# Kernel tuning notes

Measured on AMD Instinct MI355X. Metric: run time of the kernel, lower is better.

Reference implementation:

```python
import jax, jax.numpy as jnp
import numpy as np

DMODEL = 1024
NUM_HEADS = 16
HEAD_DIM = DMODEL // NUM_HEADS


def setup_inputs() -> dict:
    key = jax.random.key(0)
    k_x, k_wqkv, k_bqkv, k_wo, k_bo = jax.random.split(key, 5)
    B, T, D = 4, 2048, DMODEL
    s = 1.0 / np.sqrt(D)
    return {
        "x": jax.random.normal(k_x, (B, T, D), dtype=jnp.float32),
        "w_qkv": jax.random.uniform(k_wqkv, (D, 3 * D), dtype=jnp.float32, minval=-s, maxval=s),
        "b_qkv": jax.random.uniform(k_bqkv, (3 * D,), dtype=jnp.float32, minval=-s, maxval=s),
        "w_out": jax.random.uniform(k_wo, (D, D), dtype=jnp.float32, minval=-s, maxval=s),
        "b_out": jax.random.uniform(k_bo, (D,), dtype=jnp.float32, minval=-s, maxval=s),
    }


def reference(x, w_qkv, b_qkv, w_out, b_out):
    B, T, D = x.shape
    H, Hd = NUM_HEADS, HEAD_DIM
    qkv = x @ w_qkv + b_qkv                      # [B,T,3D]
    qkv = qkv.reshape(B, T, 3, H, Hd)
    q = jnp.transpose(qkv[:, :, 0], (0, 2, 1, 3))  # [B,H,T,Hd]
    k = jnp.transpose(qkv[:, :, 1], (0, 2, 1, 3))
    v = jnp.transpose(qkv[:, :, 2], (0, 2, 1, 3))
    scores = jnp.einsum("bhqd,bhkd->bhqk", q, k) / jnp.sqrt(jnp.float32(Hd))
    weights = jax.nn.softmax(scores, axis=-1)
    attn = jnp.einsum("bhqk,bhkd->bhqd", weights, v)  # [B,H,T,Hd]
    attn = jnp.transpose(attn, (0, 2, 1, 3)).reshape(B, T, D)
    return attn @ w_out + b_out
```

## Files before the change

kernel.cpp:

```cpp
#include <hip/hip_runtime.h>
#include <hip/hip_bf16.h>


typedef __bf16 bf16_t;
typedef __bf16 bf16x8 __attribute__((ext_vector_type(8)));
typedef float f32x4 __attribute__((ext_vector_type(4)));
typedef short short4v __attribute__((ext_vector_type(4)));

#if __has_builtin(__builtin_amdgcn_mfma_f32_16x16x16_bf16)
typedef __bf16 bf16x4 __attribute__((ext_vector_type(4)));
#define MFMA_PV(va, vb, c) __builtin_amdgcn_mfma_f32_16x16x16_bf16( \
    __builtin_bit_cast(bf16x4, (va)), __builtin_bit_cast(bf16x4, (vb)), (c), 0, 0, 0)
#else
#define MFMA_PV(va, vb, c) __builtin_amdgcn_mfma_f32_16x16x16bf16_1k((va), (vb), (c), 0, 0, 0)
#endif

#define DMODEL 1024
#define NH     16
#define HD     64
#define BATCH  4
#define SEQ    2048
#define NTOK   (BATCH * SEQ)
#define NOUT   (NTOK * DMODEL)
#define CEXP   0.1803368801111204f

__device__ __forceinline__ void async_ld16(void* lds, const void* g) {
  __builtin_amdgcn_global_load_lds(
      (const __attribute__((address_space(1))) void*)g,
      (__attribute__((address_space(3))) void*)lds, 16, 0, 0);
}

__global__ __launch_bounds__(256) void sniff_dtype(
    const uint4* __restrict__ x, int* __restrict__ flag) {
  int t = threadIdx.x;
  uint4 v = x[t];
  int nanish = 0, zc = 0;
  for (int j = 0; j < 4; ++j) {
    uint4 w = x[t + j * 256];
    unsigned u[4] = {w.x, w.y, w.z, w.w};
    for (int k = 0; k < 4; ++k) {
      unsigned lo = u[k] & 0xFFFFu, hi = u[k] >> 16;
      if ((lo & 0x7F80u) == 0x7F80u) nanish++;
      if ((hi & 0x7F80u) == 0x7F80u) nanish++;
      if (lo == 0) zc++;
      if (hi == 0) zc++;
    }
  }
  (void)v;
  __shared__ int rn[256], rz[256];
  rn[t] = nanish; rz[t] = zc;
  __syncthreads();
  for (int s = 128; s > 0; s >>= 1) {
    if (t < s) { rn[t] += rn[t + s]; rz[t] += rz[t + s]; }
    __syncthreads();
  }
  if (t == 0) flag[0] = (rn[0] > 4 || rz[0] > 2048) ? 1 : 0;
}

__global__ __launch_bounds__(256) void conv_to_bf16(
    const void* __restrict__ src, bf16_t* __restrict__ dst, int n,
    const int* __restrict__ flag) {
  int i = (blockIdx.x * 256 + threadIdx.x) * 8;
  if (i >= n) return;
  if (flag[0]) {
    const float4* s = (const float4*)((const float*)src + i);
    float4 a = s[0], b = s[1];
    bf16_t* o = dst + i;
    o[0] = (bf16_t)a.x; o[1] = (bf16_t)a.y; o[2] = (bf16_t)a.z; o[3] = (bf16_t)a.w;
    o[4] = (bf16_t)b.x; o[5] = (bf16_t)b.y; o[6] = (bf16_t)b.z; o[7] = (bf16_t)b.w;
  } else {
    *(uint4*)(dst + i) = *(const uint4*)((const bf16_t*)src + i);
  }
}

__global__ __launch_bounds__(256) void conv_biases(
    const void* __restrict__ sq, const void* __restrict__ so,
    float* __restrict__ dq, float* __restrict__ dofs,
    const int* __restrict__ flag) {
  int i = blockIdx.x * 256 + threadIdx.x;
  if (i < 3072)
    dq[i] = flag[0] ? ((const float*)sq)[i] : (float)((const bf16_t*)sq)[i];
  else {
    int j = i - 3072;
    dofs[j] = flag[0] ? ((const float*)so)[j] : (float)((const bf16_t*)so)[j];
  }
}

__global__ __launch_bounds__(256) void transpose_w(
    const void* __restrict__ in, bf16_t* __restrict__ out, int R, int C,
    const int* __restrict__ flag) {
  __shared__ bf16_t tile[32][33];
  const int tx = threadIdx.x & 31, ty = threadIdx.x >> 5;
  const int c0 = blockIdx.x * 32, r0 = blockIdx.y * 32;
  if (flag[0]) {
    for (int i = 0; i < 4; ++i) {
      int r = ty + i * 8;
      tile[r][tx] = (bf16_t)((const float*)in)[(size_t)(r0 + r) * C + c0 + tx];
    }
  } else {
    for (int i = 0; i < 4; ++i) {
      int r = ty + i * 8;
      tile[r][tx] = ((const bf16_t*)in)[(size_t)(r0 + r) * C + c0 + tx];
    }
  }
  __syncthreads();
  for (int i = 0; i < 4; ++i) {
    int r = ty + i * 8;
    out[(size_t)(c0 + r) * R + r0 + tx] = tile[tx][r];
  }
}

template <int MODE>
__global__ __launch_bounds__(256) void gemm_bt_bias(
    const bf16_t* __restrict__ A, const bf16_t* __restrict__ Bt,
    const float* __restrict__ bias, void* __restrict__ Cout,
    int M, int N, int K, const int* __restrict__ flag,
    bf16_t* __restrict__ vT) {
  __shared__ bf16_t sA[128 * 32];
  __shared__ bf16_t sB[128 * 32];
  const int t = threadIdx.x;
  const int wave = t >> 6, lane = t & 63;
  const int quad = lane >> 4, l16 = lane & 15;
  const int bM = blockIdx.y * 128, bN = blockIdx.x * 128;
  const int m0w = (wave >> 1) * 64, n0w = (wave & 1) * 64;
  const int rowS = wave * 16 + (lane >> 2);
  const int kcS = (lane & 3) * 8;

  f32x4 acc[4][4] = {};

  for (int k0 = 0; k0 < K; k0 += 32) {
    for (int r = 0; r < 2; ++r) {
      int row = r * 64 + rowS;
      async_ld16((char*)sA + r * 4096 + wave * 1024,
                 A + (size_t)(bM + row) * K + k0 + kcS);
      async_ld16((char*)sB + r * 4096 + wave * 1024,
                 Bt + (size_t)(bN + row) * K + k0 + kcS);
    }
    __syncthreads();

    bf16x8 af[4], bfr[4];
    for (int i = 0; i < 4; ++i)
      af[i] = *(const bf16x8*)&sA[(m0w + i * 16 + l16) * 32 + quad * 8];
    for (int j = 0; j < 4; ++j)
      bfr[j] = *(const bf16x8*)&sB[(n0w + j * 16 + l16) * 32 + quad * 8];
    for (int i = 0; i < 4; ++i)
      for (int j = 0; j < 4; ++j)
        acc[i][j] = __builtin_amdgcn_mfma_f32_16x16x32_bf16(af[i], bfr[j], acc[i][j], 0, 0, 0);
    __syncthreads();
  }

  const bool f32out = (MODE == 1) && flag[0];
  for (int j = 0; j < 4; ++j) {
    int col = bN + n0w + j * 16 + l16;
    float bv = bias[col];
    for (int i = 0; i < 4; ++i) {
      int row0 = bM + m0w + i * 16 + quad * 4;
      if (MODE == 2 && col >= 2048) {
        int hh = (col - 2048) >> 6, dd = (col - 2048) & 63;
        bf16_t o4[4];
        for (int r = 0; r < 4; ++r) o4[r] = (bf16_t)(acc[i][j][r] + bv);
        size_t dst = ((((size_t)(row0 >> 11) * NH + hh) * HD + dd) << 11) | (row0 & 2047);
        *(uint2*)&vT[dst] = *(uint2*)o4;
      } else {
        float scale = (MODE == 2 && col < 1024) ? CEXP : 1.0f;
        for (int r = 0; r < 4; ++r) {
          float v = (acc[i][j][r] + bv) * scale;
          if (f32out) ((float*)Cout)[(size_t)(row0 + r) * N + col] = v;
          else        ((bf16_t*)Cout)[(size_t)(row0 + r) * N + col] = (bf16_t)v;
        }
      }
    }
  }
}

__global__ __launch_bounds__(512) void attention_v9(
    const bf16_t* __restrict__ qkv, const bf16_t* __restrict__ vT,
    bf16_t* __restrict__ attn) {
  const int t = threadIdx.x;
  const int wave = t >> 6, lane = t & 63;
  const int quad = lane >> 4, l16 = lane & 15;
  const int bh = blockIdx.x, b = bh >> 4, h = bh & 15;
  const int qw = blockIdx.y * 256 + wave * 32;

  __shared__ bf16_t Kt[2][128 * 64];
  __shared__ bf16_t Vt[2][64 * 128];

  const bf16_t* qglob = qkv + (size_t)b * SEQ * 3072 + h * 64;
  const bf16_t* kglob = qglob + 1024;
  const bf16_t* vglob = vT + (size_t)bh * HD * SEQ;

  bf16x8 qf[2][2];
  for (int s = 0; s < 2; ++s) {
    const bf16_t* qrow = qglob + (size_t)(qw + s * 16 + l16) * 3072 + quad * 8;
    qf[s][0] = *(const bf16x8*)qrow;
    qf[s][1] = *(const bf16x8*)(qrow + 32);
  }

  f32x4 accO[2][4] = {};
  float lpart[2] = {0.f, 0.f};

  const int kRow = lane >> 3, kSlot = lane & 7;
  const int vRow = lane >> 4, vSlot = lane & 15;

  auto stageKV = [&](int buf, int kt) {
    for (int j = 0; j < 2; ++j) {
      int keyl = wave * 16 + j * 8 + kRow;
      int gc = kSlot ^ (keyl & 7);
      async_ld16((char*)Kt[buf] + (wave * 16 + j * 8) * 128,
                 kglob + (size_t)(kt + keyl) * 3072 + gc * 8);
    }
    for (int j = 0; j < 2; ++j) {
      int d = wave * 8 + j * 4 + vRow;
      int gc = vSlot ^ (d & 15);
      async_ld16((char*)Vt[buf] + (wave * 8 + j * 4) * 256,
                 vglob + (size_t)d * SEQ + kt + gc * 8);
    }
  };

  stageKV(0, 0);

  for (int ti = 0; ti < SEQ / 128; ++ti) {
    const int buf = ti & 1;
    __syncthreads();
    if (ti + 1 < SEQ / 128) stageKV(buf ^ 1, (ti + 1) * 128);

    const bf16_t* KtB = Kt[buf];
    const bf16_t* VtB = Vt[buf];

    for (int kb = 0; kb < 8; ++kb) {
      const bf16_t* kr = &KtB[(kb * 16 + l16) * 64];
      bf16x8 kf0 = *(const bf16x8*)(kr + ((quad ^ (l16 & 7)) * 8));
      bf16x8 kf1 = *(const bf16x8*)(kr + (((4 + quad) ^ (l16 & 7)) * 8));

      short4v pB[2];
      for (int s = 0; s < 2; ++s) {
        f32x4 z = {0.f, 0.f, 0.f, 0.f};
        f32x4 st = __builtin_amdgcn_mfma_f32_16x16x32_bf16(kf0, qf[s][0], z, 0, 0, 0);
        st = __builtin_amdgcn_mfma_f32_16x16x32_bf16(kf1, qf[s][1], st, 0, 0, 0);
        union { bf16_t hh[4]; short4v s4; } u;
        for (int r = 0; r < 4; ++r) {
          float p = __builtin_amdgcn_exp2f(st[r]);
          lpart[s] += p;
          u.hh[r] = (bf16_t)p;
        }
        pB[s] = u.s4;
      }

      const int chunkbase = kb * 2 + (quad >> 1);
      const int coff = (quad & 1) * 4;
      for (int db = 0; db < 4; ++db) {
        short4v vf = *(const short4v*)&VtB[(db * 16 + l16) * 128 +
                                           ((chunkbase ^ l16) * 8) + coff];
        for (int s = 0; s < 2; ++s)
          accO[s][db] = MFMA_PV(vf, pB[s], accO[s][db]);
      }
    }
  }

  for (int s = 0; s < 2; ++s) {
    float l = lpart[s];
    l += __shfl_xor(l, 16);
    l += __shfl_xor(l, 32);
    float inv = 1.f / l;
    size_t tok = (size_t)b * SEQ + qw + s * 16 + l16;
    for (int db = 0; db < 4; ++db) {
      bf16_t o4[4];
      for (int r = 0; r < 4; ++r) o4[r] = (bf16_t)(accO[s][db][r] * inv);
      *(uint2*)&attn[tok * DMODEL + h * HD + db * 16 + quad * 4] = *(uint2*)o4;
    }
  }
}

extern "C" void kernel_launch(void* const* d_in, const int* in_sizes, int n_in,
                              void* d_out, int out_size, void* d_ws, size_t ws_size,
                              hipStream_t stream) {
  const void* x     = d_in[0];
  const void* w_qkv = d_in[1];
  const void* b_qkv = d_in[2];
  const void* w_out = d_in[3];
  const void* b_out = d_in[4];

  char* ws = (char*)d_ws;
  int*    flag  = (int*)ws;
  bf16_t* wqkvT = (bf16_t*)(ws + 4096);
  bf16_t* woutT = (bf16_t*)(ws + 6295552);
  float*  bqkvf = (float*)(ws + 8392704);
  float*  boutf = (float*)(ws + 8404992);
  bf16_t* qkv   = (bf16_t*)(ws + 8409088);
  bf16_t* xb    = (bf16_t*)(ws + 58740736);
  bf16_t* attn  = xb;
  bf16_t* vTbuf = (bf16_t*)(ws + 75517952);

  sniff_dtype<<<1, 256, 0, stream>>>((const uint4*)x, flag);

  conv_to_bf16<<<NOUT / 2048, 256, 0, stream>>>(x, xb, NOUT, flag);
  conv_biases<<<16, 256, 0, stream>>>(b_qkv, b_out, bqkvf, boutf, flag);

  transpose_w<<<dim3(96, 32), 256, 0, stream>>>(w_qkv, wqkvT, 1024, 3072, flag);
  transpose_w<<<dim3(32, 32), 256, 0, stream>>>(w_out, woutT, 1024, 1024, flag);

  gemm_bt_bias<2><<<dim3(24, 64), 256, 0, stream>>>(
      xb, wqkvT, bqkvf, qkv, NTOK, 3072, 1024, flag, vTbuf);

  attention_v9<<<dim3(BATCH * NH, SEQ / 256), 512, 0, stream>>>(qkv, vTbuf, attn);

  gemm_bt_bias<1><<<dim3(8, 64), 256, 0, stream>>>(
      attn, woutT, boutf, d_out, NTOK, 1024, 1024, flag, nullptr);
}
```

Measured before the change: 295.4 us.

## Software-pipeline QK and PV MFMAs in attention and swizzle GEMM block order

The attention inner loop is restructured so the QK^T scores for the next key block are computed while the exp and PV MFMAs of the current block run. Each wave starts at a different key sub-block to spread LDS bank traffic, s_setprio is raised around the PV MFMAs, and the row-sum is kept in four independent partial accumulators. Separately, the GEMM remaps workgroup IDs into eight strided groups, presumably to match XCD placement and improve L2 reuse. The pipelining costs extra registers, which could hurt occupancy.

```diff
diff --git a/kernel.cpp b/kernel.cpp
--- a/kernel.cpp
+++ b/kernel.cpp
@@ -121,7 +121,12 @@
   const int t = threadIdx.x;
   const int wave = t >> 6, lane = t & 63;
   const int quad = lane >> 4, l16 = lane & 15;
-  const int bM = blockIdx.y * 128, bN = blockIdx.x * 128;
+  const int nwg = gridDim.x * gridDim.y;
+  const int lin = blockIdx.y * gridDim.x + blockIdx.x;
+  const int cpx = nwg >> 3;
+  const int swz = (lin & 7) * cpx + (lin >> 3);
+  const int bx = swz % gridDim.x, by = swz / gridDim.x;
+  const int bM = by * 128, bN = bx * 128;
   const int m0w = (wave >> 1) * 64, n0w = (wave & 1) * 64;
   const int rowS = wave * 16 + (lane >> 2);
   const int kcS = (lane & 3) * 8;
@@ -173,7 +178,7 @@
   }
 }
 
-__global__ __launch_bounds__(512) void attention_v9(
+__global__ __launch_bounds__(512) void attention_v10(
     const bf16_t* __restrict__ qkv, const bf16_t* __restrict__ vT,
     bf16_t* __restrict__ attn) {
   const int t = threadIdx.x;
@@ -197,7 +202,7 @@
   }
 
   f32x4 accO[2][4] = {};
-  float lpart[2] = {0.f, 0.f};
+  f32x4 lp[2] = {};
 
   const int kRow = lane >> 3, kSlot = lane & 7;
   const int vRow = lane >> 4, vSlot = lane & 15;
@@ -219,6 +224,8 @@
 
   stageKV(0, 0);
 
+  const int kb0 = wave & 7;
+
   for (int ti = 0; ti < SEQ / 128; ++ti) {
     const int buf = ti & 1;
     __syncthreads();
@@ -227,38 +234,62 @@
     const bf16_t* KtB = Kt[buf];
     const bf16_t* VtB = Vt[buf];
 
-    for (int kb = 0; kb < 8; ++kb) {
-      const bf16_t* kr = &KtB[(kb * 16 + l16) * 64];
-      bf16x8 kf0 = *(const bf16x8*)(kr + ((quad ^ (l16 & 7)) * 8));
-      bf16x8 kf1 = *(const bf16x8*)(kr + (((4 + quad) ^ (l16 & 7)) * 8));
-
+    f32x4 stc[2];
+    {
+      const bf16_t* kr = &KtB[(kb0 * 16 + l16) * 64];
+      bf16x8 a = *(const bf16x8*)(kr + ((quad ^ (l16 & 7)) * 8));
+      bf16x8 c = *(const bf16x8*)(kr + (((4 + quad) ^ (l16 & 7)) * 8));
+      for (int s = 0; s < 2; ++s) {
+        f32x4 z = {0.f, 0.f, 0.f, 0.f};
+        stc[s] = __builtin_amdgcn_mfma_f32_16x16x32_bf16(a, qf[s][0], z, 0, 0, 0);
+        stc[s] = __builtin_amdgcn_mfma_f32_16x16x32_bf16(c, qf[s][1], stc[s], 0, 0, 0);
+      }
+    }
+
+#pragma unroll
+    for (int i = 0; i < 8; ++i) {
+      const int kbc = (kb0 + i) & 7;
+      bf16x8 an, cn;
+      if (i < 7) {
+        const int kbn = (kb0 + i + 1) & 7;
+        const bf16_t* kr = &KtB[(kbn * 16 + l16) * 64];
+        an = *(const bf16x8*)(kr + ((quad ^ (l16 & 7)) * 8));
+        cn = *(const bf16x8*)(kr + (((4 + quad) ^ (l16 & 7)) * 8));
+      }
       short4v pB[2];
       for (int s = 0; s < 2; ++s) {
-        f32x4 z = {0.f, 0.f, 0.f, 0.f};
-        f32x4 st = __builtin_amdgcn_mfma_f32_16x16x32_bf16(kf0, qf[s][0], z, 0, 0, 0);
-        st = __builtin_amdgcn_mfma_f32_16x16x32_bf16(kf1, qf[s][1], st, 0, 0, 0);
         union { bf16_t hh[4]; short4v s4; } u;
         for (int r = 0; r < 4; ++r) {
-          float p = __builtin_amdgcn_exp2f(st[r]);
-          lpart[s] += p;
+          float p = __builtin_amdgcn_exp2f(stc[s][r]);
+          lp[s][r] += p;
           u.hh[r] = (bf16_t)p;
         }
         pB[s] = u.s4;
       }
-
-      const int chunkbase = kb * 2 + (quad >> 1);
+      f32x4 stn[2];
+      if (i < 7) {
+        for (int s = 0; s < 2; ++s) {
+          f32x4 z = {0.f, 0.f, 0.f, 0.f};
+          stn[s] = __builtin_amdgcn_mfma_f32_16x16x32_bf16(an, qf[s][0], z, 0, 0, 0);
+          stn[s] = __builtin_amdgcn_mfma_f32_16x16x32_bf16(cn, qf[s][1], stn[s], 0, 0, 0);
+        }
+      }
+      const int chunkbase = kbc * 2 + (quad >> 1);
       const int coff = (quad & 1) * 4;
+      __builtin_amdgcn_s_setprio(1);
       for (int db = 0; db < 4; ++db) {
         short4v vf = *(const short4v*)&VtB[(db * 16 + l16) * 128 +
                                            ((chunkbase ^ l16) * 8) + coff];
         for (int s = 0; s < 2; ++s)
           accO[s][db] = MFMA_PV(vf, pB[s], accO[s][db]);
       }
+      __builtin_amdgcn_s_setprio(0);
+      if (i < 7) { stc[0] = stn[0]; stc[1] = stn[1]; }
     }
   }
 
   for (int s = 0; s < 2; ++s) {
-    float l = lpart[s];
+    float l = (lp[s][0] + lp[s][1]) + (lp[s][2] + lp[s][3]);
     l += __shfl_xor(l, 16);
     l += __shfl_xor(l, 32);
     float inv = 1.f / l;
@@ -302,7 +333,7 @@
   gemm_bt_bias<2><<<dim3(24, 64), 256, 0, stream>>>(
       xb, wqkvT, bqkvf, qkv, NTOK, 3072, 1024, flag, vTbuf);
 
-  attention_v9<<<dim3(BATCH * NH, SEQ / 256), 512, 0, stream>>>(qkv, vTbuf, attn);
+  attention_v10<<<dim3(BATCH * NH, SEQ / 256), 512, 0, stream>>>(qkv, vTbuf, attn);
 
   gemm_bt_bias<1><<<dim3(8, 64), 256, 0, stream>>>(
       attn, woutT, boutf, d_out, NTOK, 1024, 1024, flag, nullptr);
```

New measurement: 311.9 us. 1.06x slower.

## Drop LDS staging in attention, read K/V directly; add XCD-aware block swizzles

Applied to the files above, without the earlier changes.

The attention kernel no longer stages K and V tiles through double-buffered shared memory with barriers. Each wave now loads its K and V fragments straight from global memory, relying on L2 and the per-XCD caches. Blocks are remapped so that each XCD handles eight heads, and the GEMM grid gets a similar XCD swizzle, to improve cache locality across MI355X's chiplets. The per-row partial sums are also split into four accumulators. This removes sync and LDS traffic, but every wave now loads K/V redundantly from global memory and depends on cache hits.

```diff
diff --git a/kernel.cpp b/kernel.cpp
--- a/kernel.cpp
+++ b/kernel.cpp
@@ -121,7 +121,12 @@
   const int t = threadIdx.x;
   const int wave = t >> 6, lane = t & 63;
   const int quad = lane >> 4, l16 = lane & 15;
-  const int bM = blockIdx.y * 128, bN = blockIdx.x * 128;
+  const int nwg = gridDim.x * gridDim.y;
+  const int lin = blockIdx.y * gridDim.x + blockIdx.x;
+  const int cpx = nwg >> 3;
+  const int swz = (lin & 7) * cpx + (lin >> 3);
+  const int bx = swz % gridDim.x, by = swz / gridDim.x;
+  const int bM = by * 128, bN = bx * 128;
   const int m0w = (wave >> 1) * 64, n0w = (wave & 1) * 64;
   const int rowS = wave * 16 + (lane >> 2);
   const int kcS = (lane & 3) * 8;
@@ -173,17 +178,18 @@
   }
 }
 
-__global__ __launch_bounds__(512) void attention_v9(
+__global__ __launch_bounds__(512) void attention_v11(
     const bf16_t* __restrict__ qkv, const bf16_t* __restrict__ vT,
     bf16_t* __restrict__ attn) {
   const int t = threadIdx.x;
   const int wave = t >> 6, lane = t & 63;
   const int quad = lane >> 4, l16 = lane & 15;
-  const int bh = blockIdx.x, b = bh >> 4, h = bh & 15;
-  const int qw = blockIdx.y * 256 + wave * 32;
-
-  __shared__ bf16_t Kt[2][128 * 64];
-  __shared__ bf16_t Vt[2][64 * 128];
+  const int lin = blockIdx.y * gridDim.x + blockIdx.x;
+  const int xcd = lin & 7, j = lin >> 3;
+  const int bh = xcd * 8 + (j & 7);
+  const int qy = j >> 3;
+  const int b = bh >> 4, h = bh & 15;
+  const int qw = qy * 256 + wave * 32;
 
   const bf16_t* qglob = qkv + (size_t)b * SEQ * 3072 + h * 64;
   const bf16_t* kglob = qglob + 1024;
@@ -197,68 +203,43 @@
   }
 
   f32x4 accO[2][4] = {};
-  float lpart[2] = {0.f, 0.f};
-
-  const int kRow = lane >> 3, kSlot = lane & 7;
-  const int vRow = lane >> 4, vSlot = lane & 15;
-
-  auto stageKV = [&](int buf, int kt) {
-    for (int j = 0; j < 2; ++j) {
-      int keyl = wave * 16 + j * 8 + kRow;
-      int gc = kSlot ^ (keyl & 7);
-      async_ld16((char*)Kt[buf] + (wave * 16 + j * 8) * 128,
-                 kglob + (size_t)(kt + keyl) * 3072 + gc * 8);
-    }
-    for (int j = 0; j < 2; ++j) {
-      int d = wave * 8 + j * 4 + vRow;
-      int gc = vSlot ^ (d & 15);
-      async_ld16((char*)Vt[buf] + (wave * 8 + j * 4) * 256,
-                 vglob + (size_t)d * SEQ + kt + gc * 8);
-    }
-  };
-
-  stageKV(0, 0);
-
-  for (int ti = 0; ti < SEQ / 128; ++ti) {
-    const int buf = ti & 1;
-    __syncthreads();
-    if (ti + 1 < SEQ / 128) stageKV(buf ^ 1, (ti + 1) * 128);
-
-    const bf16_t* KtB = Kt[buf];
-    const bf16_t* VtB = Vt[buf];
-
-    for (int kb = 0; kb < 8; ++kb) {
-      const bf16_t* kr = &KtB[(kb * 16 + l16) * 64];
-      bf16x8 kf0 = *(const bf16x8*)(kr + ((quad ^ (l16 & 7)) * 8));
-      bf16x8 kf1 = *(const bf16x8*)(kr + (((4 + quad) ^ (l16 & 7)) * 8));
-
-      short4v pB[2];
-      for (int s = 0; s < 2; ++s) {
-        f32x4 z = {0.f, 0.f, 0.f, 0.f};
-        f32x4 st = __builtin_amdgcn_mfma_f32_16x16x32_bf16(kf0, qf[s][0], z, 0, 0, 0);
-        st = __builtin_amdgcn_mfma_f32_16x16x32_bf16(kf1, qf[s][1], st, 0, 0, 0);
-        union { bf16_t hh[4]; short4v s4; } u;
-        for (int r = 0; r < 4; ++r) {
-          float p = __builtin_amdgcn_exp2f(st[r]);
-          lpart[s] += p;
-          u.hh[r] = (bf16_t)p;
-        }
-        pB[s] = u.s4;
+  f32x4 lp[2] = {};
+
+  const bf16_t* krow = kglob + (size_t)l16 * 3072 + quad * 8;
+  const bf16_t* vrow = vglob + (size_t)l16 * SEQ + quad * 4;
+
+#pragma unroll 2
+  for (int kk = 0; kk < SEQ; kk += 16) {
+    bf16x8 kf0 = *(const bf16x8*)(krow);
+    bf16x8 kf1 = *(const bf16x8*)(krow + 32);
+    short4v vf[4];
+    for (int db = 0; db < 4; ++db)
+      vf[db] = *(const short4v*)(vrow + (size_t)db * 16 * SEQ);
+
+    short4v pB[2];
+    for (int s = 0; s < 2; ++s) {
+      f32x4 z = {0.f, 0.f, 0.f, 0.f};
+      f32x4 st = __builtin_amdgcn_mfma_f32_16x16x32_bf16(kf0, qf[s][0], z, 0, 0, 0);
+      st = __builtin_amdgcn_mfma_f32_16x16x32_bf16(kf1, qf[s][1], st, 0, 0, 0);
+      union { bf16_t hh[4]; short4v s4; } u;
+      for (int r = 0; r < 4; ++r) {
+        float p = __builtin_amdgcn_exp2f(st[r]);
+        lp[s][r] += p;
+        u.hh[r] = (bf16_t)p;
       }
-
-      const int chunkbase = kb * 2 + (quad >> 1);
-      const int coff = (quad & 1) * 4;
-      for (int db = 0; db < 4; ++db) {
-        short4v vf = *(const short4v*)&VtB[(db * 16 + l16) * 128 +
-                                           ((chunkbase ^ l16) * 8) + coff];
-        for (int s = 0; s < 2; ++s)
-          accO[s][db] = MFMA_PV(vf, pB[s], accO[s][db]);
-      }
-    }
+      pB[s] = u.s4;
+    }
+
+    for (int db = 0; db < 4; ++db)
+      for (int s = 0; s < 2; ++s)
+        accO[s][db] = MFMA_PV(vf[db], pB[s], accO[s][db]);
+
+    krow += 16 * 3072;
+    vrow += 16;
   }
 
   for (int s = 0; s < 2; ++s) {
-    float l = lpart[s];
+    float l = (lp[s][0] + lp[s][1]) + (lp[s][2] + lp[s][3]);
     l += __shfl_xor(l, 16);
     l += __shfl_xor(l, 32);
     float inv = 1.f / l;
@@ -302,7 +283,7 @@
   gemm_bt_bias<2><<<dim3(24, 64), 256, 0, stream>>>(
       xb, wqkvT, bqkvf, qkv, NTOK, 3072, 1024, flag, vTbuf);
 
-  attention_v9<<<dim3(BATCH * NH, SEQ / 256), 512, 0, stream>>>(qkv, vTbuf, attn);
+  attention_v11<<<dim3(BATCH * NH, SEQ / 256), 512, 0, stream>>>(qkv, vTbuf, attn);
 
   gemm_bt_bias<1><<<dim3(8, 64), 256, 0, stream>>>(
       attn, woutT, boutf, d_out, NTOK, 1024, 1024, flag, nullptr);
```

New measurement: 546.2 us. +84.9%, slower.

## Double-buffer GEMM LDS staging, swizzle workgroup order, split softmax row-sum accumulators

Applied to the files above, without the earlier changes.

The bias GEMM now double-buffers its LDS tiles. It issues async loads for the next K-step before computing the current one, and uses a partial vmcnt wait with raw barriers, so global loads overlap the MFMA work. Workgroup IDs are remapped in groups of 8 to improve L2 locality across neighbouring tiles. In attention, the softmax denominator uses four independent accumulators to break the serial add dependency chain. This doubles GEMM LDS use, which may lower occupancy, and relies on the vmcnt(4) count matching the number of loads issued per stage.

```diff
diff --git a/kernel.cpp b/kernel.cpp
--- a/kernel.cpp
+++ b/kernel.cpp
@@ -116,37 +116,58 @@
     const float* __restrict__ bias, void* __restrict__ Cout,
     int M, int N, int K, const int* __restrict__ flag,
     bf16_t* __restrict__ vT) {
-  __shared__ bf16_t sA[128 * 32];
-  __shared__ bf16_t sB[128 * 32];
+  __shared__ bf16_t sA[2][128 * 32];
+  __shared__ bf16_t sB[2][128 * 32];
   const int t = threadIdx.x;
   const int wave = t >> 6, lane = t & 63;
   const int quad = lane >> 4, l16 = lane & 15;
-  const int bM = blockIdx.y * 128, bN = blockIdx.x * 128;
+  const int nwg = gridDim.x * gridDim.y;
+  const int lin = blockIdx.y * gridDim.x + blockIdx.x;
+  const int cpx = nwg >> 3;
+  const int swz = (lin & 7) * cpx + (lin >> 3);
+  const int bx = swz % gridDim.x, by = swz / gridDim.x;
+  const int bM = by * 128, bN = bx * 128;
   const int m0w = (wave >> 1) * 64, n0w = (wave & 1) * 64;
   const int rowS = wave * 16 + (lane >> 2);
   const int kcS = (lane & 3) * 8;
 
   f32x4 acc[4][4] = {};
 
-  for (int k0 = 0; k0 < K; k0 += 32) {
+  auto stage = [&](int buf, int k0) {
     for (int r = 0; r < 2; ++r) {
       int row = r * 64 + rowS;
-      async_ld16((char*)sA + r * 4096 + wave * 1024,
+      async_ld16((char*)sA[buf] + r * 4096 + wave * 1024,
                  A + (size_t)(bM + row) * K + k0 + kcS);
-      async_ld16((char*)sB + r * 4096 + wave * 1024,
+      async_ld16((char*)sB[buf] + r * 4096 + wave * 1024,
                  Bt + (size_t)(bN + row) * K + k0 + kcS);
     }
-    __syncthreads();
+  };
+
+  const int nsteps = K >> 5;
+  stage(0, 0);
+
+  for (int s = 0; s < nsteps; ++s) {
+    const int cur = s & 1;
+    if (s + 1 < nsteps) {
+      stage(cur ^ 1, (s + 1) << 5);
+      asm volatile("s_waitcnt vmcnt(4)" ::: "memory");
+    } else {
+      asm volatile("s_waitcnt vmcnt(0)" ::: "memory");
+    }
+    __builtin_amdgcn_s_barrier();
+    asm volatile("" ::: "memory");
 
     bf16x8 af[4], bfr[4];
     for (int i = 0; i < 4; ++i)
-      af[i] = *(const bf16x8*)&sA[(m0w + i * 16 + l16) * 32 + quad * 8];
+      af[i] = *(const bf16x8*)&sA[cur][(m0w + i * 16 + l16) * 32 + quad * 8];
     for (int j = 0; j < 4; ++j)
-      bfr[j] = *(const bf16x8*)&sB[(n0w + j * 16 + l16) * 32 + quad * 8];
+      bfr[j] = *(const bf16x8*)&sB[cur][(n0w + j * 16 + l16) * 32 + quad * 8];
     for (int i = 0; i < 4; ++i)
       for (int j = 0; j < 4; ++j)
         acc[i][j] = __builtin_amdgcn_mfma_f32_16x16x32_bf16(af[i], bfr[j], acc[i][j], 0, 0, 0);
-    __syncthreads();
+
+    asm volatile("" ::: "memory");
+    __builtin_amdgcn_s_barrier();
   }
 
   const bool f32out = (MODE == 1) && flag[0];
@@ -197,7 +218,7 @@
   }
 
   f32x4 accO[2][4] = {};
-  float lpart[2] = {0.f, 0.f};
+  f32x4 lp[2] = {};
 
   const int kRow = lane >> 3, kSlot = lane & 7;
   const int vRow = lane >> 4, vSlot = lane & 15;
@@ -240,7 +261,7 @@
         union { bf16_t hh[4]; short4v s4; } u;
         for (int r = 0; r < 4; ++r) {
           float p = __builtin_amdgcn_exp2f(st[r]);
-          lpart[s] += p;
+          lp[s][r] += p;
           u.hh[r] = (bf16_t)p;
         }
         pB[s] = u.s4;
@@ -258,7 +279,7 @@
   }
 
   for (int s = 0; s < 2; ++s) {
-    float l = lpart[s];
+    float l = (lp[s][0] + lp[s][1]) + (lp[s][2] + lp[s][3]);
     l += __shfl_xor(l, 16);
     l += __shfl_xor(l, 32);
     float inv = 1.f / l;
```

Result: slower. 302.2 us (+2.3%).
